# Kernel tuning notes

Measured on AMD Instinct MI355X. Metric: run time of the kernel, lower is better.

## Reference

```python
import jax, jax.numpy as jnp
import numpy as np

EMBED_DIM = 512
NUM_HEADS = 8
HEAD_DIM = EMBED_DIM // NUM_HEADS
SCALE = HEAD_DIM ** -0.5
TEMP = 1.0


def setup_inputs() -> dict:
    key = jax.random.key(0)
    ks = jax.random.split(key, 12)
    B, N, Nk, C = 4, 2048, 2048, EMBED_DIM
    s = C ** -0.5
    return {
        "x": jax.random.normal(ks[0], (B, N, C), jnp.float32),
        "y": jax.random.normal(ks[1], (B, Nk, C), jnp.float32),
        "z": jax.random.normal(ks[2], (B, Nk, C), jnp.float32),
        "Wq": jax.random.normal(ks[3], (C, C), jnp.float32) * s,
        "bq": jnp.zeros((C,), jnp.float32),
        "Wk": jax.random.normal(ks[4], (C, C), jnp.float32) * s,
        "bk": jnp.zeros((C,), jnp.float32),
        "Wv": jax.random.normal(ks[5], (C, C), jnp.float32) * s,
        "bv": jnp.zeros((C,), jnp.float32),
        "Wo": jax.random.normal(ks[6], (C, C), jnp.float32) * s,
        "bo": jnp.zeros((C,), jnp.float32),
    }


def reference(x, y, z, Wq, bq, Wk, bk, Wv, bv, Wo, bo):
    B, N, C = x.shape
    Nk = y.shape[1]
    H, D = NUM_HEADS, HEAD_DIM

    def split_heads(t, L):
        return t.reshape(B, L, H, D).transpose(0, 2, 1, 3)  # [B,H,L,D]

    q = split_heads(x @ Wq.T + bq, N)
    k = split_heads(y @ Wk.T + bk, Nk)
    v = split_heads(z @ Wv.T + bv, Nk)

    # [B,H,N,Nk] logits, scaled
    logits = jnp.einsum("bhnd,bhkd->bhnk", q, k) * SCALE

    # Gumbel-softmax (soft, tau=TEMP) with a fixed noise key
    gkey = jax.random.key(42)
    gumbels = jax.random.gumbel(gkey, logits.shape, logits.dtype)
    attn = jax.nn.softmax((logits + gumbels) / TEMP, axis=-1)

    out = jnp.einsum("bhnk,bhkd->bhnd", attn, v)
    out = out.transpose(0, 2, 1, 3).reshape(B, N, C)
    return out @ Wo.T + bo
```

## Files before the change

### kernel.cpp

```cpp
#include <hip/hip_runtime.h>
#include <hip/hip_bf16.h>
#include <stdint.h>

#define Bdim 4
#define Hdim 8
#define Ndim 2048
#define Cdim 512
#define Ddim 64
#define SCALE_F 0.125f
#define KSPLIT 4
#define LOG2E 1.44269504f

typedef __bf16 bf16_t;
typedef __bf16 bf16x8 __attribute__((ext_vector_type(8)));
typedef float f32x4 __attribute__((ext_vector_type(4)));

#define SWZ_XOR_F(v, m) \
  __int_as_float(__builtin_amdgcn_ds_swizzle(__float_as_int(v), (0x1F | ((m) << 10))))

__device__ __forceinline__ float gumbel_pfac(uint32_t flat) {
  const uint32_t k0 = 0u, k1 = 42u, k2 = 0x1BD11BDAu ^ 0u ^ 42u;
  uint32_t x0 = 0u;
  uint32_t x1 = flat;
  x0 += k0; x1 += k1;
#define TF_R(r) { x0 += x1; x1 = __builtin_rotateleft32(x1, r); x1 ^= x0; }
#define TF_R4A TF_R(13) TF_R(15) TF_R(26) TF_R(6)
#define TF_R4B TF_R(17) TF_R(29) TF_R(16) TF_R(24)
  TF_R4A  x0 += k1; x1 += k2 + 1u;
  TF_R4B  x0 += k2; x1 += k0 + 2u;
  TF_R4A  x0 += k0; x1 += k1 + 3u;
  TF_R4B  x0 += k1; x1 += k2 + 4u;
  TF_R4A  x0 += k2; x1 += k0 + 5u;
#undef TF_R4B
#undef TF_R4A
#undef TF_R
  uint32_t bits = x0 ^ x1;
  float f = __uint_as_float((bits >> 9) | 0x3F800000u) - 1.0f;
  float u = f + 1.17549435e-38f;
  return -__builtin_amdgcn_rcpf(__builtin_amdgcn_logf(u));
}

__global__ void cvt_f32_bf16(const float* __restrict__ in,
                             bf16_t* __restrict__ out, int n8) {
  int i = blockIdx.x * blockDim.x + threadIdx.x;
  if (i < n8) {
    const float4* p = (const float4*)in + (size_t)i * 2;
    float4 a = p[0], b = p[1];
    union { bf16_t h[8]; uint4 u; } pk;
    pk.h[0] = (bf16_t)a.x; pk.h[1] = (bf16_t)a.y;
    pk.h[2] = (bf16_t)a.z; pk.h[3] = (bf16_t)a.w;
    pk.h[4] = (bf16_t)b.x; pk.h[5] = (bf16_t)b.y;
    pk.h[6] = (bf16_t)b.z; pk.h[7] = (bf16_t)b.w;
    *((uint4*)out + i) = pk.u;
  }
}

__device__ __forceinline__ void gemm_core(const bf16_t* __restrict__ A,
                                          const bf16_t* __restrict__ W,
                                          int m0, int n0,
                                          bf16_t* As, bf16_t* Ws,
                                          f32x4 (&acc)[4][4]) {
  const int t = threadIdx.x;
  const int wave = t >> 6, lane = t & 63;
  const int ln = lane & 15, qd = lane >> 4;
  const int wm = wave >> 1, wn = wave & 1;

#pragma unroll
  for (int i = 0; i < 4; i++)
#pragma unroll
    for (int j = 0; j < 4; j++) acc[i][j] = (f32x4){0.f, 0.f, 0.f, 0.f};

  for (int kt = 0; kt < Cdim / 64; ++kt) {
#pragma unroll
    for (int it = 0; it < 4; ++it) {
      int vec = it * 256 + t;
      int row = vec >> 3, c8 = (vec & 7) * 8;
      *(bf16x8*)&As[row * 72 + c8] =
          *(const bf16x8*)&A[(size_t)(m0 + row) * Cdim + kt * 64 + c8];
      *(bf16x8*)&Ws[row * 72 + c8] =
          *(const bf16x8*)&W[(size_t)(n0 + row) * Cdim + kt * 64 + c8];
    }
    __syncthreads();
#pragma unroll
    for (int ks = 0; ks < 2; ++ks) {
      bf16x8 af[4], bfr[4];
#pragma unroll
      for (int i = 0; i < 4; i++)
        af[i] = *(const bf16x8*)&As[(wm * 64 + i * 16 + ln) * 72 + ks * 32 + qd * 8];
#pragma unroll
      for (int j = 0; j < 4; j++)
        bfr[j] = *(const bf16x8*)&Ws[(wn * 64 + j * 16 + ln) * 72 + ks * 32 + qd * 8];
#pragma unroll
      for (int i = 0; i < 4; i++)
#pragma unroll
        for (int j = 0; j < 4; j++)
          acc[i][j] = __builtin_amdgcn_mfma_f32_16x16x32_bf16(af[i], bfr[j],
                                                              acc[i][j], 0, 0, 0);
    }
    __syncthreads();
  }
}

__global__ __launch_bounds__(256, 2)
void qkv_gemm_kernel(const bf16_t* __restrict__ xb, const bf16_t* __restrict__ yb,
                     const bf16_t* __restrict__ zb, const bf16_t* __restrict__ wqb,
                     const bf16_t* __restrict__ wkb, const bf16_t* __restrict__ wvb,
                     const float* __restrict__ bq, const float* __restrict__ bk,
                     const float* __restrict__ bv, bf16_t* __restrict__ qo,
                     bf16_t* __restrict__ ko, bf16_t* __restrict__ vo) {
  __shared__ bf16_t As[128 * 72];
  __shared__ bf16_t Ws[128 * 72];
  const int sel = blockIdx.z;
  const bf16_t* A = sel == 0 ? xb : (sel == 1 ? yb : zb);
  const bf16_t* W = sel == 0 ? wqb : (sel == 1 ? wkb : wvb);
  const float* bias = sel == 0 ? bq : (sel == 1 ? bk : bv);
  bf16_t* O = sel == 0 ? qo : (sel == 1 ? ko : vo);
  const float mul = sel == 0 ? SCALE_F : 1.0f;
  const int m0 = blockIdx.y * 128, n0 = blockIdx.x * 128;

  f32x4 acc[4][4];
  gemm_core(A, W, m0, n0, As, Ws, acc);

  const int t = threadIdx.x;
  const int wave = t >> 6, lane = t & 63;
  const int ln = lane & 15, qd = lane >> 4;
  const int wm = wave >> 1, wn = wave & 1;
#pragma unroll
  for (int i = 0; i < 4; i++)
#pragma unroll
    for (int j = 0; j < 4; j++)
#pragma unroll
      for (int r = 0; r < 4; r++) {
        int grow = m0 + wm * 64 + i * 16 + qd * 4 + r;
        int gcol = n0 + wn * 64 + j * 16 + ln;
        float val = (acc[i][j][r] + bias[gcol]) * mul;
        int b = grow >> 11, n = grow & 2047;
        int h = gcol >> 6, d = gcol & 63;
        O[(((size_t)b * Hdim + h) * Ndim + n) * Ddim + d] = (bf16_t)val;
      }
}

__global__ __launch_bounds__(256, 2)
void out_gemm_kernel(const bf16_t* __restrict__ ab, const bf16_t* __restrict__ wob,
                     const float* __restrict__ bo, float* __restrict__ out) {
  __shared__ bf16_t As[128 * 72];
  __shared__ bf16_t Ws[128 * 72];
  const int m0 = blockIdx.y * 128, n0 = blockIdx.x * 128;
  f32x4 acc[4][4];
  gemm_core(ab, wob, m0, n0, As, Ws, acc);

  const int t = threadIdx.x;
  const int wave = t >> 6, lane = t & 63;
  const int ln = lane & 15, qd = lane >> 4;
  const int wm = wave >> 1, wn = wave & 1;
#pragma unroll
  for (int i = 0; i < 4; i++)
#pragma unroll
    for (int j = 0; j < 4; j++)
#pragma unroll
      for (int r = 0; r < 4; r++) {
        int grow = m0 + wm * 64 + i * 16 + qd * 4 + r;
        int gcol = n0 + wn * 64 + j * 16 + ln;
        out[(size_t)grow * Cdim + gcol] = acc[i][j][r] + bo[gcol];
      }
}

__global__ __launch_bounds__(256, 4)
void attn_kernel(const bf16_t* __restrict__ qb, const bf16_t* __restrict__ kb,
                 const bf16_t* __restrict__ vb, bf16_t* __restrict__ part_o,
                 float* __restrict__ part_l) {
  __shared__ bf16_t Ks[64 * 72];
  __shared__ bf16_t Vt[64 * 72];
  __shared__ bf16_t Ps[64 * 72];

  const int t = threadIdx.x;
  const int wave = t >> 6, lane = t & 63;
  const int ln = lane & 15, qd = lane >> 4;
  const int qtile = blockIdx.x;
  const int bh = blockIdx.y;
  const int z = blockIdx.z;
  const int qbase = qtile * 64;
  const int kt_lo = z * (Ndim / 64 / KSPLIT);
  const int kt_hi = kt_lo + (Ndim / 64 / KSPLIT);

  const bf16_t* Qg = qb + (size_t)bh * Ndim * Ddim;
  const bf16_t* Kg = kb + (size_t)bh * Ndim * Ddim;
  const bf16_t* Vg = vb + (size_t)bh * Ndim * Ddim;

  const bf16_t* Qrow = Qg + (size_t)(qbase + wave * 16 + ln) * Ddim;
  bf16x8 qf0 = *(const bf16x8*)&Qrow[qd * 8];
  bf16x8 qf1 = *(const bf16x8*)&Qrow[32 + qd * 8];

  const int row0 = t >> 3,        c80 = (t & 7) * 8;
  const int row1 = (256 + t) >> 3, c81 = ((256 + t) & 7) * 8;
  const int swz0 = ((row0 >> 3) ^ (c80 >> 3)) * 8 + (row0 & 7);
  const int swz1 = ((row1 >> 3) ^ (c81 >> 3)) * 8 + (row1 & 7);

  bf16x8 kr0 = *(const bf16x8*)&Kg[(size_t)(kt_lo * 64 + row0) * Ddim + c80];
  bf16x8 kr1 = *(const bf16x8*)&Kg[(size_t)(kt_lo * 64 + row1) * Ddim + c81];
  bf16x8 vr0 = *(const bf16x8*)&Vg[(size_t)(kt_lo * 64 + row0) * Ddim + c80];
  bf16x8 vr1 = *(const bf16x8*)&Vg[(size_t)(kt_lo * 64 + row1) * Ddim + c81];

  float l_r[4] = {0.f, 0.f, 0.f, 0.f};
  f32x4 o_acc[4];
#pragma unroll
  for (int j = 0; j < 4; j++) o_acc[j] = (f32x4){0.f, 0.f, 0.f, 0.f};

  const uint32_t flat_bh = (uint32_t)bh << 22;

  for (int kt = kt_lo; kt < kt_hi; ++kt) {
    *(bf16x8*)&Ks[row0 * 72 + c80] = kr0;
    *(bf16x8*)&Ks[row1 * 72 + c81] = kr1;
#pragma unroll
    for (int jj = 0; jj < 8; jj++) Vt[(c80 + jj) * 72 + swz0] = vr0[jj];
#pragma unroll
    for (int jj = 0; jj < 8; jj++) Vt[(c81 + jj) * 72 + swz1] = vr1[jj];
    __syncthreads();

    if (kt + 1 < kt_hi) {
      kr0 = *(const bf16x8*)&Kg[(size_t)((kt + 1) * 64 + row0) * Ddim + c80];
      kr1 = *(const bf16x8*)&Kg[(size_t)((kt + 1) * 64 + row1) * Ddim + c81];
      vr0 = *(const bf16x8*)&Vg[(size_t)((kt + 1) * 64 + row0) * Ddim + c80];
      vr1 = *(const bf16x8*)&Vg[(size_t)((kt + 1) * 64 + row1) * Ddim + c81];
    }

    f32x4 s[4];
#pragma unroll
    for (int j = 0; j < 4; j++) s[j] = (f32x4){0.f, 0.f, 0.f, 0.f};
#pragma unroll
    for (int j = 0; j < 4; j++) {
      bf16x8 bk0 = *(const bf16x8*)&Ks[(j * 16 + ln) * 72 + qd * 8];
      bf16x8 bk1 = *(const bf16x8*)&Ks[(j * 16 + ln) * 72 + 32 + qd * 8];
      s[j] = __builtin_amdgcn_mfma_f32_16x16x32_bf16(qf0, bk0, s[j], 0, 0, 0);
      s[j] = __builtin_amdgcn_mfma_f32_16x16x32_bf16(qf1, bk1, s[j], 0, 0, 0);
    }

#pragma unroll
    for (int r = 0; r < 4; r++) {
      int qrow = qbase + wave * 16 + qd * 4 + r;
      uint32_t fbase = flat_bh + ((uint32_t)qrow << 11) + (uint32_t)(kt * 64 + ln);
#pragma unroll
      for (int j = 0; j < 4; j++) {
        float pf = gumbel_pfac(fbase + j * 16);
        float pv = __builtin_amdgcn_exp2f(s[j][r] * LOG2E) * pf;
        l_r[r] += pv;
        Ps[(wave * 16 + qd * 4 + r) * 72 + j * 16 + ln] = (bf16_t)pv;
      }
    }

#pragma unroll
    for (int ks = 0; ks < 2; ++ks) {
      bf16x8 af = *(const bf16x8*)&Ps[(wave * 16 + ln) * 72 + ks * 32 + qd * 8];
#pragma unroll
      for (int j = 0; j < 4; j++) {
        int d = j * 16 + ln;
        bf16x8 bv8 = *(const bf16x8*)&Vt[d * 72 + (((ks * 4 + qd) ^ (d >> 3)) << 3)];
        o_acc[j] = __builtin_amdgcn_mfma_f32_16x16x32_bf16(af, bv8, o_acc[j], 0, 0, 0);
      }
    }
    __syncthreads();
  }

  const int pidx = ((bh << 5) | qtile) * KSPLIT + z;
  bf16_t* po = part_o + (size_t)pidx * 64 * 64;
  float* pl = part_l + (size_t)pidx * 64;

#pragma unroll
  for (int r = 0; r < 4; r++) {
    float lsum = l_r[r];
    lsum += SWZ_XOR_F(lsum, 1);
    lsum += SWZ_XOR_F(lsum, 2);
    lsum += SWZ_XOR_F(lsum, 4);
    lsum += SWZ_XOR_F(lsum, 8);
    if (ln == 0) pl[wave * 16 + qd * 4 + r] = lsum;
  }
#pragma unroll
  for (int j = 0; j < 4; j++)
#pragma unroll
    for (int r = 0; r < 4; r++) {
      int row = wave * 16 + qd * 4 + r;
      int col = j * 16 + ln;
      po[row * 64 + col] = (bf16_t)o_acc[j][r];
    }
}

__global__ __launch_bounds__(256, 8)
void attn_combine(const bf16_t* __restrict__ part_o,
                  const float* __restrict__ part_l, bf16_t* __restrict__ ab) {
  const int blk = blockIdx.x;
  const int bh = blk >> 5, qtile = blk & 31;
  const int t = threadIdx.x;
  const int row = t >> 2, c0 = (t & 3) * 16;

  float l = 0.f;
#pragma unroll
  for (int zz = 0; zz < KSPLIT; zz++)
    l += part_l[(size_t)(blk * KSPLIT + zz) * 64 + row];
  const float linv = 1.0f / l;

  float acc[16];
#pragma unroll
  for (int i = 0; i < 16; i++) acc[i] = 0.f;
#pragma unroll
  for (int zz = 0; zz < KSPLIT; zz++) {
    const bf16_t* po =
        part_o + (size_t)(blk * KSPLIT + zz) * 64 * 64 + row * 64 + c0;
    bf16x8 a0 = *(const bf16x8*)&po[0];
    bf16x8 a1 = *(const bf16x8*)&po[8];
#pragma unroll
    for (int i = 0; i < 8; i++) { acc[i] += (float)a0[i]; acc[8 + i] += (float)a1[i]; }
  }

  const int b = bh >> 3, h = bh & 7;
  bf16_t* dst = ab + ((size_t)b * Ndim + qtile * 64 + row) * Cdim + h * 64 + c0;
  union { bf16_t h8[8]; uint4 u; } pk0, pk1;
#pragma unroll
  for (int i = 0; i < 8; i++) {
    pk0.h8[i] = (bf16_t)(acc[i] * linv);
    pk1.h8[i] = (bf16_t)(acc[8 + i] * linv);
  }
  *(uint4*)&dst[0] = pk0.u;
  *(uint4*)&dst[8] = pk1.u;
}

extern "C" void kernel_launch(void* const* d_in, const int* in_sizes, int n_in,
                              void* d_out, int out_size, void* d_ws, size_t ws_size,
                              hipStream_t stream) {
  const float* x  = (const float*)d_in[0];
  const float* y  = (const float*)d_in[1];
  const float* z  = (const float*)d_in[2];
  const float* Wq = (const float*)d_in[3];
  const float* bq = (const float*)d_in[4];
  const float* Wk = (const float*)d_in[5];
  const float* bk = (const float*)d_in[6];
  const float* Wv = (const float*)d_in[7];
  const float* bv = (const float*)d_in[8];
  const float* Wo = (const float*)d_in[9];
  const float* bo = (const float*)d_in[10];
  float* out = (float*)d_out;

  bf16_t* base = (bf16_t*)d_ws;
  const size_t NBIG = (size_t)Bdim * Ndim * Cdim;
  const size_t NW   = (size_t)Cdim * Cdim;
  bf16_t* xb  = base;
  bf16_t* yb  = xb + NBIG;
  bf16_t* zb  = yb + NBIG;
  bf16_t* wqb = zb + NBIG;
  bf16_t* wkb = wqb + NW;
  bf16_t* wvb = wkb + NW;
  bf16_t* wob = wvb + NW;
  bf16_t* qb  = wob + NW;
  bf16_t* kb  = qb + NBIG;
  bf16_t* vb  = kb + NBIG;
  bf16_t* ab  = vb + NBIG;
  bf16_t* part_o = ab + NBIG;
  float* part_l = (float*)(part_o + (size_t)1024 * KSPLIT * 64 * 64);

  int n8b = (int)(NBIG / 8), n8w = (int)(NW / 8);
  cvt_f32_bf16<<<n8b / 256, 256, 0, stream>>>(x, xb, n8b);
  cvt_f32_bf16<<<n8b / 256, 256, 0, stream>>>(y, yb, n8b);
  cvt_f32_bf16<<<n8b / 256, 256, 0, stream>>>(z, zb, n8b);
  cvt_f32_bf16<<<n8w / 256, 256, 0, stream>>>(Wq, wqb, n8w);
  cvt_f32_bf16<<<n8w / 256, 256, 0, stream>>>(Wk, wkb, n8w);
  cvt_f32_bf16<<<n8w / 256, 256, 0, stream>>>(Wv, wvb, n8w);
  cvt_f32_bf16<<<n8w / 256, 256, 0, stream>>>(Wo, wob, n8w);

  qkv_gemm_kernel<<<dim3(Cdim / 128, (Bdim * Ndim) / 128, 3), 256, 0, stream>>>(
      xb, yb, zb, wqb, wkb, wvb, bq, bk, bv, qb, kb, vb);

  attn_kernel<<<dim3(Ndim / 64, Bdim * Hdim, KSPLIT), 256, 0, stream>>>(
      qb, kb, vb, part_o, part_l);

  attn_combine<<<dim3(1024), 256, 0, stream>>>(part_o, part_l, ab);

  out_gemm_kernel<<<dim3(Cdim / 128, (Bdim * Ndim) / 128), 256, 0, stream>>>(
      ab, wob, bo, out);
}
```

Before: 440.5 us.

## Fuse fp32-to-bf16 conversion into GEMM loads and read K fragments from global

Removes the seven standalone fp32-to-bf16 conversion kernels. The QKV and output GEMMs now load fp32 inputs and weights directly and convert them while staging into LDS, which avoids writing and re-reading the bf16 copies. The attention kernel also drops the K shared-memory tile: each wave loads its K MFMA fragments straight from global memory every iteration, saving LDS traffic but adding redundant global reads across the four waves and exposing that load latency without prefetch.

```diff
diff --git a/kernel.cpp b/kernel.cpp
--- a/kernel.cpp
+++ b/kernel.cpp
@@ -40,23 +40,23 @@
   return -__builtin_amdgcn_rcpf(__builtin_amdgcn_logf(u));
 }
 
-__global__ void cvt_f32_bf16(const float* __restrict__ in,
-                             bf16_t* __restrict__ out, int n8) {
-  int i = blockIdx.x * blockDim.x + threadIdx.x;
-  if (i < n8) {
-    const float4* p = (const float4*)in + (size_t)i * 2;
-    float4 a = p[0], b = p[1];
-    union { bf16_t h[8]; uint4 u; } pk;
-    pk.h[0] = (bf16_t)a.x; pk.h[1] = (bf16_t)a.y;
-    pk.h[2] = (bf16_t)a.z; pk.h[3] = (bf16_t)a.w;
-    pk.h[4] = (bf16_t)b.x; pk.h[5] = (bf16_t)b.y;
-    pk.h[6] = (bf16_t)b.z; pk.h[7] = (bf16_t)b.w;
-    *((uint4*)out + i) = pk.u;
-  }
-}
-
-__device__ __forceinline__ void gemm_core(const bf16_t* __restrict__ A,
-                                          const bf16_t* __restrict__ W,
+__device__ __forceinline__ void stage8(bf16_t* dst, const bf16_t* src) {
+  *(uint4*)dst = *(const uint4*)src;
+}
+__device__ __forceinline__ void stage8(bf16_t* dst, const float* src) {
+  const float4* p = (const float4*)src;
+  float4 a = p[0], b = p[1];
+  union { bf16_t h[8]; uint4 u; } pk;
+  pk.h[0] = (bf16_t)a.x; pk.h[1] = (bf16_t)a.y;
+  pk.h[2] = (bf16_t)a.z; pk.h[3] = (bf16_t)a.w;
+  pk.h[4] = (bf16_t)b.x; pk.h[5] = (bf16_t)b.y;
+  pk.h[6] = (bf16_t)b.z; pk.h[7] = (bf16_t)b.w;
+  *(uint4*)dst = pk.u;
+}
+
+template <typename TA, typename TW>
+__device__ __forceinline__ void gemm_core(const TA* __restrict__ A,
+                                          const TW* __restrict__ W,
                                           int m0, int n0,
                                           bf16_t* As, bf16_t* Ws,
                                           f32x4 (&acc)[4][4]) {
@@ -75,10 +75,8 @@
     for (int it = 0; it < 4; ++it) {
       int vec = it * 256 + t;
       int row = vec >> 3, c8 = (vec & 7) * 8;
-      *(bf16x8*)&As[row * 72 + c8] =
-          *(const bf16x8*)&A[(size_t)(m0 + row) * Cdim + kt * 64 + c8];
-      *(bf16x8*)&Ws[row * 72 + c8] =
-          *(const bf16x8*)&W[(size_t)(n0 + row) * Cdim + kt * 64 + c8];
+      stage8(&As[row * 72 + c8], &A[(size_t)(m0 + row) * Cdim + kt * 64 + c8]);
+      stage8(&Ws[row * 72 + c8], &W[(size_t)(n0 + row) * Cdim + kt * 64 + c8]);
     }
     __syncthreads();
 #pragma unroll
@@ -102,17 +100,17 @@
 }
 
 __global__ __launch_bounds__(256, 2)
-void qkv_gemm_kernel(const bf16_t* __restrict__ xb, const bf16_t* __restrict__ yb,
-                     const bf16_t* __restrict__ zb, const bf16_t* __restrict__ wqb,
-                     const bf16_t* __restrict__ wkb, const bf16_t* __restrict__ wvb,
+void qkv_gemm_kernel(const float* __restrict__ x, const float* __restrict__ y,
+                     const float* __restrict__ z, const float* __restrict__ Wq,
+                     const float* __restrict__ Wk, const float* __restrict__ Wv,
                      const float* __restrict__ bq, const float* __restrict__ bk,
                      const float* __restrict__ bv, bf16_t* __restrict__ qo,
                      bf16_t* __restrict__ ko, bf16_t* __restrict__ vo) {
   __shared__ bf16_t As[128 * 72];
   __shared__ bf16_t Ws[128 * 72];
   const int sel = blockIdx.z;
-  const bf16_t* A = sel == 0 ? xb : (sel == 1 ? yb : zb);
-  const bf16_t* W = sel == 0 ? wqb : (sel == 1 ? wkb : wvb);
+  const float* A = sel == 0 ? x : (sel == 1 ? y : z);
+  const float* W = sel == 0 ? Wq : (sel == 1 ? Wk : Wv);
   const float* bias = sel == 0 ? bq : (sel == 1 ? bk : bv);
   bf16_t* O = sel == 0 ? qo : (sel == 1 ? ko : vo);
   const float mul = sel == 0 ? SCALE_F : 1.0f;
@@ -141,13 +139,13 @@
 }
 
 __global__ __launch_bounds__(256, 2)
-void out_gemm_kernel(const bf16_t* __restrict__ ab, const bf16_t* __restrict__ wob,
+void out_gemm_kernel(const bf16_t* __restrict__ ab, const float* __restrict__ Wo,
                      const float* __restrict__ bo, float* __restrict__ out) {
   __shared__ bf16_t As[128 * 72];
   __shared__ bf16_t Ws[128 * 72];
   const int m0 = blockIdx.y * 128, n0 = blockIdx.x * 128;
   f32x4 acc[4][4];
-  gemm_core(ab, wob, m0, n0, As, Ws, acc);
+  gemm_core(ab, Wo, m0, n0, As, Ws, acc);
 
   const int t = threadIdx.x;
   const int wave = t >> 6, lane = t & 63;
@@ -169,7 +167,6 @@
 void attn_kernel(const bf16_t* __restrict__ qb, const bf16_t* __restrict__ kb,
                  const bf16_t* __restrict__ vb, bf16_t* __restrict__ part_o,
                  float* __restrict__ part_l) {
-  __shared__ bf16_t Ks[64 * 72];
   __shared__ bf16_t Vt[64 * 72];
   __shared__ bf16_t Ps[64 * 72];
 
@@ -191,13 +188,11 @@
   bf16x8 qf0 = *(const bf16x8*)&Qrow[qd * 8];
   bf16x8 qf1 = *(const bf16x8*)&Qrow[32 + qd * 8];
 
-  const int row0 = t >> 3,        c80 = (t & 7) * 8;
+  const int row0 = t >> 3,         c80 = (t & 7) * 8;
   const int row1 = (256 + t) >> 3, c81 = ((256 + t) & 7) * 8;
   const int swz0 = ((row0 >> 3) ^ (c80 >> 3)) * 8 + (row0 & 7);
   const int swz1 = ((row1 >> 3) ^ (c81 >> 3)) * 8 + (row1 & 7);
 
-  bf16x8 kr0 = *(const bf16x8*)&Kg[(size_t)(kt_lo * 64 + row0) * Ddim + c80];
-  bf16x8 kr1 = *(const bf16x8*)&Kg[(size_t)(kt_lo * 64 + row1) * Ddim + c81];
   bf16x8 vr0 = *(const bf16x8*)&Vg[(size_t)(kt_lo * 64 + row0) * Ddim + c80];
   bf16x8 vr1 = *(const bf16x8*)&Vg[(size_t)(kt_lo * 64 + row1) * Ddim + c81];
 
@@ -209,8 +204,14 @@
   const uint32_t flat_bh = (uint32_t)bh << 22;
 
   for (int kt = kt_lo; kt < kt_hi; ++kt) {
-    *(bf16x8*)&Ks[row0 * 72 + c80] = kr0;
-    *(bf16x8*)&Ks[row1 * 72 + c81] = kr1;
+    const bf16_t* Kt = Kg + (size_t)(kt * 64 + ln) * Ddim + qd * 8;
+    bf16x8 bk0[4], bk1[4];
+#pragma unroll
+    for (int j = 0; j < 4; j++) {
+      bk0[j] = *(const bf16x8*)&Kt[j * 16 * Ddim];
+      bk1[j] = *(const bf16x8*)&Kt[j * 16 * Ddim + 32];
+    }
+
 #pragma unroll
     for (int jj = 0; jj < 8; jj++) Vt[(c80 + jj) * 72 + swz0] = vr0[jj];
 #pragma unroll
@@ -218,8 +219,6 @@
     __syncthreads();
 
     if (kt + 1 < kt_hi) {
-      kr0 = *(const bf16x8*)&Kg[(size_t)((kt + 1) * 64 + row0) * Ddim + c80];
-      kr1 = *(const bf16x8*)&Kg[(size_t)((kt + 1) * 64 + row1) * Ddim + c81];
       vr0 = *(const bf16x8*)&Vg[(size_t)((kt + 1) * 64 + row0) * Ddim + c80];
       vr1 = *(const bf16x8*)&Vg[(size_t)((kt + 1) * 64 + row1) * Ddim + c81];
     }
@@ -229,10 +228,8 @@
     for (int j = 0; j < 4; j++) s[j] = (f32x4){0.f, 0.f, 0.f, 0.f};
 #pragma unroll
     for (int j = 0; j < 4; j++) {
-      bf16x8 bk0 = *(const bf16x8*)&Ks[(j * 16 + ln) * 72 + qd * 8];
-      bf16x8 bk1 = *(const bf16x8*)&Ks[(j * 16 + ln) * 72 + 32 + qd * 8];
-      s[j] = __builtin_amdgcn_mfma_f32_16x16x32_bf16(qf0, bk0, s[j], 0, 0, 0);
-      s[j] = __builtin_amdgcn_mfma_f32_16x16x32_bf16(qf1, bk1, s[j], 0, 0, 0);
+      s[j] = __builtin_amdgcn_mfma_f32_16x16x32_bf16(qf0, bk0[j], s[j], 0, 0, 0);
+      s[j] = __builtin_amdgcn_mfma_f32_16x16x32_bf16(qf1, bk1[j], s[j], 0, 0, 0);
     }
 
 #pragma unroll
@@ -341,32 +338,15 @@
 
   bf16_t* base = (bf16_t*)d_ws;
   const size_t NBIG = (size_t)Bdim * Ndim * Cdim;
-  const size_t NW   = (size_t)Cdim * Cdim;
-  bf16_t* xb  = base;
-  bf16_t* yb  = xb + NBIG;
-  bf16_t* zb  = yb + NBIG;
-  bf16_t* wqb = zb + NBIG;
-  bf16_t* wkb = wqb + NW;
-  bf16_t* wvb = wkb + NW;
-  bf16_t* wob = wvb + NW;
-  bf16_t* qb  = wob + NW;
+  bf16_t* qb  = base;
   bf16_t* kb  = qb + NBIG;
   bf16_t* vb  = kb + NBIG;
   bf16_t* ab  = vb + NBIG;
   bf16_t* part_o = ab + NBIG;
   float* part_l = (float*)(part_o + (size_t)1024 * KSPLIT * 64 * 64);
 
-  int n8b = (int)(NBIG / 8), n8w = (int)(NW / 8);
-  cvt_f32_bf16<<<n8b / 256, 256, 0, stream>>>(x, xb, n8b);
-  cvt_f32_bf16<<<n8b / 256, 256, 0, stream>>>(y, yb, n8b);
-  cvt_f32_bf16<<<n8b / 256, 256, 0, stream>>>(z, zb, n8b);
-  cvt_f32_bf16<<<n8w / 256, 256, 0, stream>>>(Wq, wqb, n8w);
-  cvt_f32_bf16<<<n8w / 256, 256, 0, stream>>>(Wk, wkb, n8w);
-  cvt_f32_bf16<<<n8w / 256, 256, 0, stream>>>(Wv, wvb, n8w);
-  cvt_f32_bf16<<<n8w / 256, 256, 0, stream>>>(Wo, wob, n8w);
-
   qkv_gemm_kernel<<<dim3(Cdim / 128, (Bdim * Ndim) / 128, 3), 256, 0, stream>>>(
-      xb, yb, zb, wqb, wkb, wvb, bq, bk, bv, qb, kb, vb);
+      x, y, z, Wq, Wk, Wv, bq, bk, bv, qb, kb, vb);
 
   attn_kernel<<<dim3(Ndim / 64, Bdim * Hdim, KSPLIT), 256, 0, stream>>>(
       qb, kb, vb, part_o, part_l);
@@ -374,5 +354,5 @@
   attn_combine<<<dim3(1024), 256, 0, stream>>>(part_o, part_l, ab);
 
   out_gemm_kernel<<<dim3(Cdim / 128, (Bdim * Ndim) / 128), 256, 0, stream>>>(
-      ab, wob, bo, out);
-}
+      ab, Wo, bo, out);
+}
```

After: 450.9 us. +2.4%, slower.
